# Performance work log

Hardware: AMD Instinct MI355X
Metric: run time of the kernel (lower is better)

The kernel has to match this reference:

```python
import jax, jax.numpy as jnp
import numpy as np

N, E, IN, ED, OUT = 50000, 800000, 64, 16, 64
AVG_D_LOG = 2.833  # log(avg_degree + 1), avg_degree = 16
EPS = 1e-5         # PNA std epsilon


def setup_inputs() -> dict:
    key = jax.random.key(0)
    ks = jax.random.split(key, 8)
    h = jax.random.normal(ks[0], (N, IN), jnp.float32)
    ef = jax.random.normal(ks[1], (E, ED), jnp.float32)
    snorm_n = jax.random.uniform(ks[2], (N, 1), jnp.float32)
    W_pre = jax.random.normal(ks[3], (2 * IN + ED, IN), jnp.float32) * 0.05
    b_pre = jnp.zeros((IN,), jnp.float32)
    W_post = jax.random.normal(ks[4], (13 * IN, OUT), jnp.float32) * 0.05
    b_post = jnp.zeros((OUT,), jnp.float32)
    src = jax.random.randint(ks[5], (E,), 0, N, dtype=jnp.int32).astype(jnp.int64)
    dst = jax.random.randint(ks[6], (E,), 0, N, dtype=jnp.int32).astype(jnp.int64)
    return dict(h=h, ef=ef, snorm_n=snorm_n, W_pre=W_pre, b_pre=b_pre,
                W_post=W_post, b_post=b_post, src=src, dst=dst)


def reference(h, ef, snorm_n, W_pre, b_pre, W_post, b_post, src, dst):
    # pretrans MLP (1 layer -> single linear, no activation) on per-edge concat
    z = jnp.concatenate([h[src], h[dst], ef], axis=1)      # [E, 2*IN+ED]
    msg = z @ W_pre + b_pre                                # [E, IN]

    deg = jax.ops.segment_sum(jnp.ones((E,), msg.dtype), dst, num_segments=N)  # [N]
    degc = jnp.maximum(deg, 1.0)
    has_msg = (deg > 0)[:, None]

    s = jax.ops.segment_sum(msg, dst, num_segments=N)
    mean = s / degc[:, None]
    mean_sq = jax.ops.segment_sum(msg * msg, dst, num_segments=N) / degc[:, None]
    std = jnp.sqrt(jax.nn.relu(mean_sq - mean * mean) + EPS)
    mx = jax.ops.segment_max(msg, dst, num_segments=N)
    mn = jax.ops.segment_min(msg, dst, num_segments=N)

    agg = jnp.concatenate([mean, mx, mn, std], axis=1)      # [N, 4*IN]
    agg = jnp.where(has_msg, agg, 0.0)                      # zero-in-degree nodes get 0

    logd = jnp.log(degc + 1.0)
    amp = agg * (logd / AVG_D_LOG)[:, None]                 # amplification scaler
    att = agg * (AVG_D_LOG / logd)[:, None]                 # attenuation scaler

    hcat = jnp.concatenate([h, agg, amp, att], axis=1)      # [N, 13*IN]
    out = hcat @ W_post + b_post                            # posttrans MLP (1 layer)
    out = out * snorm_n                                     # graph_norm
    return out
```

## Files before the change

kernel.cpp:

```cpp
#include <hip/hip_runtime.h>

constexpr int N_NODES = 50000;
constexpr int N_EDGES = 800000;
constexpr int IN_F = 64;
constexpr int ED_F = 16;
constexpr int OUT_F = 64;
constexpr int AGG_F = 256;
constexpr int KTOT = 832;
constexpr float AVG_D_LOG_F = 2.833f;
constexpr float EPS_F = 1e-5f;

constexpr int NB_BKT = 256;
constexpr int NODES_PER_BKT = 196;
constexpr int EPB_C = 4096;
constexpr int NBLK_C = (N_EDGES + EPB_C - 1) / EPB_C;

constexpr int AGG_WAVES = 12500;
constexpr int AGG_BLOCKS = AGG_WAVES / 4;

typedef __attribute__((ext_vector_type(8))) short short8;
typedef __attribute__((ext_vector_type(4))) float f32x4;

__device__ __forceinline__ int rfl(int v) { return __builtin_amdgcn_readfirstlane(v); }
__device__ __forceinline__ unsigned short f2bf(float f) {
    unsigned u = __float_as_uint(f);
    unsigned r = (u + 0x7FFFu + ((u >> 16) & 1u)) >> 16;
    return (unsigned short)r;
}

constexpr int P12MM_BLKS = 625;
constexpr int P12_TPB = 5;
constexpr int BKT_BLKS = 196;
constexpr int CONV_BLKS = 2500;
__global__ __launch_bounds__(256) void prep_kernel(
    const float* __restrict__ h, const float* __restrict__ Wpre, const float* __restrict__ bpre,
    const int* __restrict__ dst, const float* __restrict__ ef, const float* __restrict__ Wpost,
    unsigned short* __restrict__ P1b, float* __restrict__ P2, unsigned short* __restrict__ hb,
    int* __restrict__ bktcnt, unsigned short* __restrict__ efb,
    unsigned short* __restrict__ WT, unsigned short* __restrict__ WefT)
{
    int tid = threadIdx.x;
    if (blockIdx.x < P12MM_BLKS) {
        int lane = tid & 63;
        int li = lane & 15;
        int lg = lane >> 4;
        int w = tid >> 6;
        int col = w * 16 + li;

        short8 B1[2], B2[2];
        #pragma unroll
        for (int s = 0; s < 2; ++s) {
            short8 b1 = {}, b2 = {};
            #pragma unroll
            for (int j = 0; j < 8; ++j) {
                int k = s * 32 + (lg << 3) + j;
                b1[j] = (short)f2bf(Wpre[k * 64 + col]);
                b2[j] = (short)f2bf(Wpre[(64 + k) * 64 + col]);
            }
            B1[s] = b1; B2[s] = b2;
        }
        float bj = bpre[col];

        #pragma unroll 1
        for (int t = 0; t < P12_TPB; ++t) {
            int tile = blockIdx.x + t * P12MM_BLKS;
            int nA = tile * 16 + li;
            const float* hrow = h + (size_t)nA * IN_F;
            float4 v0 = *reinterpret_cast<const float4*>(hrow + (lg << 3));
            float4 v1 = *reinterpret_cast<const float4*>(hrow + (lg << 3) + 4);
            float4 v2 = *reinterpret_cast<const float4*>(hrow + 32 + (lg << 3));
            float4 v3 = *reinterpret_cast<const float4*>(hrow + 32 + (lg << 3) + 4);
            short8 a0, a1;
            a0[0]=(short)f2bf(v0.x); a0[1]=(short)f2bf(v0.y); a0[2]=(short)f2bf(v0.z); a0[3]=(short)f2bf(v0.w);
            a0[4]=(short)f2bf(v1.x); a0[5]=(short)f2bf(v1.y); a0[6]=(short)f2bf(v1.z); a0[7]=(short)f2bf(v1.w);
            a1[0]=(short)f2bf(v2.x); a1[1]=(short)f2bf(v2.y); a1[2]=(short)f2bf(v2.z); a1[3]=(short)f2bf(v2.w);
            a1[4]=(short)f2bf(v3.x); a1[5]=(short)f2bf(v3.y); a1[6]=(short)f2bf(v3.z); a1[7]=(short)f2bf(v3.w);

            if (w == 0) {
                *reinterpret_cast<short8*>(hb + (size_t)nA * IN_F + (lg << 3)) = a0;
                *reinterpret_cast<short8*>(hb + (size_t)nA * IN_F + 32 + (lg << 3)) = a1;
            }

            f32x4 p1a = {0.f,0.f,0.f,0.f}, p2a = {0.f,0.f,0.f,0.f};
            p1a = __builtin_amdgcn_mfma_f32_16x16x32_bf16(a0, B1[0], p1a, 0, 0, 0);
            p1a = __builtin_amdgcn_mfma_f32_16x16x32_bf16(a1, B1[1], p1a, 0, 0, 0);
            p2a = __builtin_amdgcn_mfma_f32_16x16x32_bf16(a0, B2[0], p2a, 0, 0, 0);
            p2a = __builtin_amdgcn_mfma_f32_16x16x32_bf16(a1, B2[1], p2a, 0, 0, 0);

            #pragma unroll
            for (int rr = 0; rr < 4; ++rr) {
                int node = tile * 16 + (lg << 2) + rr;
                P1b[(size_t)node * IN_F + col] = f2bf(p1a[rr]);
                P2[(size_t)node * IN_F + col] = p2a[rr] + bj;
            }
        }
    } else if (blockIdx.x < P12MM_BLKS + BKT_BLKS) {
        __shared__ int bh[NB_BKT];
        bh[tid] = 0;
        __syncthreads();
        int e0 = (blockIdx.x - P12MM_BLKS) * EPB_C;
        #pragma unroll
        for (int k = 0; k < EPB_C / 256; ++k) {
            int e = e0 + k * 256 + tid;
            if (e < N_EDGES) atomicAdd(&bh[dst[e] / NODES_PER_BKT], 1);
        }
        __syncthreads();
        if (bh[tid] > 0) atomicAdd(&bktcnt[tid], bh[tid]);
    } else {
        int cgid = (blockIdx.x - P12MM_BLKS - BKT_BLKS) * 256 + tid;
        const float4* ef4 = reinterpret_cast<const float4*>(ef);
        #pragma unroll
        for (int k = 0; k < 5; ++k) {
            int i = cgid + k * (CONV_BLKS * 256);
            float4 v = ef4[i];
            ushort4 o;
            o.x = f2bf(v.x); o.y = f2bf(v.y); o.z = f2bf(v.z); o.w = f2bf(v.w);
            *reinterpret_cast<ushort4*>(efb + (size_t)i * 4) = o;
        }
        if (cgid < OUT_F * KTOT) {
            int n = cgid / KTOT, k = cgid % KTOT;
            WT[cgid] = f2bf(Wpost[(size_t)k * OUT_F + n]);
        }
        if (cgid < 64 * 16) {
            int n = cgid >> 4, k = cgid & 15;
            WefT[cgid] = f2bf(Wpre[(128 + k) * 64 + n]);
        }
    }
}

__global__ __launch_bounds__(256) void bscan_kernel(
    const int* __restrict__ bktcnt, int* __restrict__ bkt_start, int* __restrict__ bcur)
{
    __shared__ int ws[4];
    int tid = threadIdx.x, lane = tid & 63, wv = tid >> 6;
    int v = bktcnt[tid];
    int sc = v;
    #pragma unroll
    for (int off = 1; off < 64; off <<= 1) {
        int u = __shfl_up(sc, off);
        if (lane >= off) sc += u;
    }
    if (lane == 63) ws[wv] = sc;
    __syncthreads();
    int wbase = 0;
    #pragma unroll
    for (int w = 0; w < 4; ++w) if (w < wv) wbase += ws[w];
    int ex = wbase + sc - v;
    bkt_start[tid] = ex;
    bcur[tid] = ex;
    if (tid == 255) bkt_start[256] = ex + v;
}

__global__ __launch_bounds__(256) void binC_kernel(
    const int* __restrict__ src, const int* __restrict__ dst, int* __restrict__ bcur,
    int* __restrict__ stage_e, int* __restrict__ stage_s, int* __restrict__ stage_d)
{
    __shared__ int sL[EPB_C];
    __shared__ int dL[EPB_C];
    __shared__ int bh[NB_BKT];
    __shared__ int bbase[NB_BKT];
    __shared__ int bcsr[NB_BKT];

    int tid = threadIdx.x;
    int e0 = blockIdx.x * EPB_C;

    bh[tid] = 0;
    __syncthreads();
    #pragma unroll
    for (int k = 0; k < EPB_C / 256; ++k) {
        int t = k * 256 + tid;
        int e = e0 + t;
        if (e < N_EDGES) {
            int s = src[e], d = dst[e];
            sL[t] = s; dL[t] = d;
            atomicAdd(&bh[d / NODES_PER_BKT], 1);
        }
    }
    __syncthreads();
    bbase[tid] = (bh[tid] > 0) ? atomicAdd(&bcur[tid], bh[tid]) : 0;
    bcsr[tid] = 0;
    __syncthreads();
    #pragma unroll
    for (int k = 0; k < EPB_C / 256; ++k) {
        int t = k * 256 + tid;
        int e = e0 + t;
        if (e < N_EDGES) {
            int d = dL[t];
            int b = d / NODES_PER_BKT;
            int r = atomicAdd(&bcsr[b], 1);
            int pos = bbase[b] + r;
            stage_e[pos] = e;
            stage_s[pos] = sL[t];
            stage_d[pos] = d;
        }
    }
}

__global__ __launch_bounds__(256) void binD_kernel(
    const int* __restrict__ stage_e, const int* __restrict__ stage_s,
    const int* __restrict__ stage_d, const int* __restrict__ bkt_start,
    int* __restrict__ deg, int* __restrict__ row_start, int2* __restrict__ csr2)
{
    __shared__ int cnt[NB_BKT];
    __shared__ int lofs[NODES_PER_BKT];
    __shared__ int ws[4];
    int tid = threadIdx.x, lane = tid & 63, wv = tid >> 6;
    int b = blockIdx.x;
    int nb0 = b * NODES_PER_BKT;
    cnt[tid] = 0;
    __syncthreads();
    int pbeg = bkt_start[b];
    int pend = bkt_start[b + 1];
    for (int p = pbeg + tid; p < pend; p += 256)
        atomicAdd(&cnt[stage_d[p] - nb0], 1);
    __syncthreads();
    int v = cnt[tid];
    int sc = v;
    #pragma unroll
    for (int off = 1; off < 64; off <<= 1) {
        int u = __shfl_up(sc, off);
        if (lane >= off) sc += u;
    }
    if (lane == 63) ws[wv] = sc;
    __syncthreads();
    int wbase = 0;
    #pragma unroll
    for (int w = 0; w < 4; ++w) if (w < wv) wbase += ws[w];
    int ex = wbase + sc - v;
    if (tid < NODES_PER_BKT) {
        int n = nb0 + tid;
        if (n < N_NODES) { deg[n] = v; row_start[n] = pbeg + ex; }
        lofs[tid] = pbeg + ex;
    }
    __syncthreads();
    for (int p = pbeg + tid; p < pend; p += 256) {
        int d = stage_d[p];
        int r = atomicAdd(&lofs[d - nb0], 1);
        csr2[r] = make_int2(stage_e[p], stage_s[p]);
    }
}

__global__ __launch_bounds__(256) void aggmm_kernel(
    const unsigned short* __restrict__ P1b, const float* __restrict__ P2,
    const unsigned short* __restrict__ efb, const unsigned short* __restrict__ WefT,
    const int2* __restrict__ csr2, const int* __restrict__ row_start,
    const int* __restrict__ deg, unsigned short* __restrict__ aggb)
{
    int tid = threadIdx.x;
    int lane = tid & 63;
    int lg = lane >> 4;
    int li = lane & 15;

    short8 bI0 = {}, bI1 = {};
    #pragma unroll
    for (int j = 0; j < 8; ++j) {
        int k_local = (lg << 3) + j;
        if (k_local == li)      bI0[j] = (short)0x3F80;
        if (k_local == 16 + li) bI1[j] = (short)0x3F80;
    }
    short8 bE[4];
    #pragma unroll
    for (int ct = 0; ct < 4; ++ct) {
        short8 b = {};
        if (lane < 32)
            b = *reinterpret_cast<const short8*>(WefT + (size_t)(ct * 16 + li) * 16 + (lg << 3));
        bE[ct] = b;
    }

    int wgid = rfl(blockIdx.x * 4 + (tid >> 6));

    #pragma unroll 1
    for (int nn = 0; nn < 4; ++nn) {
        int n = wgid + nn * AGG_WAVES;
        int rs = rfl(row_start[n]);
        int dg = rfl(deg[n]);
        size_t obase = (size_t)n * AGG_F + lane;

        if (dg == 0) {
            aggb[obase] = 0; aggb[obase + 64] = 0;
            aggb[obase + 128] = 0; aggb[obase + 192] = 0;
            continue;
        }

        float p2n = P2[(size_t)n * IN_F + lane];
        const float NINF = -__builtin_inff(), PINF = __builtin_inff();
        float sm[4] = {0.f, 0.f, 0.f, 0.f};
        float sq[4] = {0.f, 0.f, 0.f, 0.f};
        float mx[4] = {NINF, NINF, NINF, NINF};
        float mn[4] = {PINF, PINF, PINF, PINF};

        for (int base = 0; base < dg; base += 64) {
            int cnt = dg - base; if (cnt > 64) cnt = 64;
            int2 es = make_int2(0, 0);
            if (lane < cnt) es = csr2[rs + base + lane];
            int eid = es.x, sid = es.y;
            int nfull = cnt >> 4;

            for (int rt = 0; rt < nfull; ++rt) {
                int srcidx = rt * 16 + li;
                int s_l = __shfl(sid, srcidx);
                int e_l = __shfl(eid, srcidx);
                short8 aP0 = *reinterpret_cast<const short8*>(P1b + (size_t)s_l * IN_F + (lg << 3));
                short8 aP1 = *reinterpret_cast<const short8*>(P1b + (size_t)s_l * IN_F + 32 + (lg << 3));
                short8 aE = {};
                if (lane < 32)
                    aE = *reinterpret_cast<const short8*>(efb + (size_t)e_l * ED_F + (lg << 3));

                f32x4 c0 = {0.f,0.f,0.f,0.f}, c1 = {0.f,0.f,0.f,0.f};
                f32x4 c2 = {0.f,0.f,0.f,0.f}, c3 = {0.f,0.f,0.f,0.f};
                c0 = __builtin_amdgcn_mfma_f32_16x16x32_bf16(aP0, bI0, c0, 0, 0, 0);
                c1 = __builtin_amdgcn_mfma_f32_16x16x32_bf16(aP0, bI1, c1, 0, 0, 0);
                c2 = __builtin_amdgcn_mfma_f32_16x16x32_bf16(aP1, bI0, c2, 0, 0, 0);
                c3 = __builtin_amdgcn_mfma_f32_16x16x32_bf16(aP1, bI1, c3, 0, 0, 0);
                c0 = __builtin_amdgcn_mfma_f32_16x16x32_bf16(aE, bE[0], c0, 0, 0, 0);
                c1 = __builtin_amdgcn_mfma_f32_16x16x32_bf16(aE, bE[1], c1, 0, 0, 0);
                c2 = __builtin_amdgcn_mfma_f32_16x16x32_bf16(aE, bE[2], c2, 0, 0, 0);
                c3 = __builtin_amdgcn_mfma_f32_16x16x32_bf16(aE, bE[3], c3, 0, 0, 0);

                #pragma unroll
                for (int rr = 0; rr < 4; ++rr) {
                    float x0 = c0[rr], x1 = c1[rr], x2 = c2[rr], x3 = c3[rr];
                    sm[0] += x0; sm[1] += x1; sm[2] += x2; sm[3] += x3;
                    sq[0] = fmaf(x0, x0, sq[0]); sq[1] = fmaf(x1, x1, sq[1]);
                    sq[2] = fmaf(x2, x2, sq[2]); sq[3] = fmaf(x3, x3, sq[3]);
                    mx[0] = fmaxf(mx[0], x0); mx[1] = fmaxf(mx[1], x1);
                    mx[2] = fmaxf(mx[2], x2); mx[3] = fmaxf(mx[3], x3);
                    mn[0] = fminf(mn[0], x0); mn[1] = fminf(mn[1], x1);
                    mn[2] = fminf(mn[2], x2); mn[3] = fminf(mn[3], x3);
                }
            }

            if (cnt & 15) {
                int rowb0 = nfull * 16;
                int srcidx = rowb0 + li;
                if (srcidx >= cnt) srcidx = cnt - 1;
                int s_l = __shfl(sid, srcidx);
                int e_l = __shfl(eid, srcidx);
                short8 aP0 = *reinterpret_cast<const short8*>(P1b + (size_t)s_l * IN_F + (lg << 3));
                short8 aP1 = *reinterpret_cast<const short8*>(P1b + (size_t)s_l * IN_F + 32 + (lg << 3));
                short8 aE = {};
                if (lane < 32)
                    aE = *reinterpret_cast<const short8*>(efb + (size_t)e_l * ED_F + (lg << 3));

                f32x4 c0 = {0.f,0.f,0.f,0.f}, c1 = {0.f,0.f,0.f,0.f};
                f32x4 c2 = {0.f,0.f,0.f,0.f}, c3 = {0.f,0.f,0.f,0.f};
                c0 = __builtin_amdgcn_mfma_f32_16x16x32_bf16(aP0, bI0, c0, 0, 0, 0);
                c1 = __builtin_amdgcn_mfma_f32_16x16x32_bf16(aP0, bI1, c1, 0, 0, 0);
                c2 = __builtin_amdgcn_mfma_f32_16x16x32_bf16(aP1, bI0, c2, 0, 0, 0);
                c3 = __builtin_amdgcn_mfma_f32_16x16x32_bf16(aP1, bI1, c3, 0, 0, 0);
                c0 = __builtin_amdgcn_mfma_f32_16x16x32_bf16(aE, bE[0], c0, 0, 0, 0);
                c1 = __builtin_amdgcn_mfma_f32_16x16x32_bf16(aE, bE[1], c1, 0, 0, 0);
                c2 = __builtin_amdgcn_mfma_f32_16x16x32_bf16(aE, bE[2], c2, 0, 0, 0);
                c3 = __builtin_amdgcn_mfma_f32_16x16x32_bf16(aE, bE[3], c3, 0, 0, 0);

                int rb = rowb0 + (lg << 2);
                #pragma unroll
                for (int rr = 0; rr < 4; ++rr) {
                    bool vv = (rb + rr) < cnt;
                    float x0 = c0[rr], x1 = c1[rr], x2 = c2[rr], x3 = c3[rr];
                    float z0 = vv ? x0 : 0.f, z1 = vv ? x1 : 0.f, z2 = vv ? x2 : 0.f, z3 = vv ? x3 : 0.f;
                    sm[0] += z0; sm[1] += z1; sm[2] += z2; sm[3] += z3;
                    sq[0] = fmaf(z0, z0, sq[0]); sq[1] = fmaf(z1, z1, sq[1]);
                    sq[2] = fmaf(z2, z2, sq[2]); sq[3] = fmaf(z3, z3, sq[3]);
                    mx[0] = fmaxf(mx[0], x0); mx[1] = fmaxf(mx[1], x1);
                    mx[2] = fmaxf(mx[2], x2); mx[3] = fmaxf(mx[3], x3);
                    mn[0] = fminf(mn[0], x0); mn[1] = fminf(mn[1], x1);
                    mn[2] = fminf(mn[2], x2); mn[3] = fminf(mn[3], x3);
                }
            }
        }

        #pragma unroll
        for (int ct = 0; ct < 4; ++ct) {
            #pragma unroll
            for (int off = 16; off <= 32; off <<= 1) {
                sm[ct] += __shfl_xor(sm[ct], off);
                sq[ct] += __shfl_xor(sq[ct], off);
                mx[ct] = fmaxf(mx[ct], __shfl_xor(mx[ct], off));
                mn[ct] = fminf(mn[ct], __shfl_xor(mn[ct], off));
            }
        }
        bool s16 = (lane & 16) != 0, s32 = (lane & 32) != 0;
        float S  = s32 ? (s16 ? sm[3] : sm[2]) : (s16 ? sm[1] : sm[0]);
        float Qq = s32 ? (s16 ? sq[3] : sq[2]) : (s16 ? sq[1] : sq[0]);
        float MX = s32 ? (s16 ? mx[3] : mx[2]) : (s16 ? mx[1] : mx[0]);
        float MN = s32 ? (s16 ? mn[3] : mn[2]) : (s16 ? mn[1] : mn[0]);

        float degc = (float)dg;
        float mean_x = S / degc;
        float sd = sqrtf(fmaxf(Qq / degc - mean_x * mean_x, 0.f) + EPS_F);
        aggb[obase]       = f2bf(mean_x + p2n);
        aggb[obase + 64]  = f2bf(MX + p2n);
        aggb[obase + 128] = f2bf(MN + p2n);
        aggb[obase + 192] = f2bf(sd);
    }
}

constexpr int POST_BLOCKS = 625;
constexpr int TILES_PER_BLOCK = 5;
__global__ __launch_bounds__(256, 2) void postmm_kernel(
    const unsigned short* __restrict__ hb, const float* __restrict__ snorm,
    const unsigned short* __restrict__ WT, const float* __restrict__ bpost,
    const unsigned short* __restrict__ aggb, const int* __restrict__ deg,
    float* __restrict__ out)
{
    int tid = threadIdx.x;
    int lane = tid & 63;
    int li = lane & 15;
    int lg = lane >> 4;
    int w = tid >> 6;

    const unsigned short* Brow = WT + (size_t)(w * 16 + li) * KTOT + (lg << 3);
    short8 B[26];
    #pragma unroll
    for (int s = 0; s < 26; ++s)
        B[s] = *reinterpret_cast<const short8*>(Brow + s * 32);

    float bp = bpost[w * 16 + li];

    #pragma unroll 1
    for (int t = 0; t < TILES_PER_BLOCK; ++t) {
        int tile = blockIdx.x + t * POST_BLOCKS;
        int nA = tile * 16 + li;
        const unsigned short* Ah = hb + (size_t)nA * IN_F + (lg << 3);
        const unsigned short* Ag = aggb + (size_t)nA * AGG_F + (lg << 3);

        short8 ah0 = *reinterpret_cast<const short8*>(Ah);
        short8 ah1 = *reinterpret_cast<const short8*>(Ah + 32);
        short8 ag[8];
        #pragma unroll
        for (int s = 0; s < 8; ++s)
            ag[s] = *reinterpret_cast<const short8*>(Ag + s * 32);

        f32x4 accA = {0.f,0.f,0.f,0.f}, accB = {0.f,0.f,0.f,0.f}, accC = {0.f,0.f,0.f,0.f};
        accA = __builtin_amdgcn_mfma_f32_16x16x32_bf16(ah0, B[0], accA, 0, 0, 0);
        accA = __builtin_amdgcn_mfma_f32_16x16x32_bf16(ah1, B[1], accA, 0, 0, 0);
        #pragma unroll
        for (int s = 0; s < 8; ++s) {
            accA = __builtin_amdgcn_mfma_f32_16x16x32_bf16(ag[s], B[2 + s],  accA, 0, 0, 0);
            accB = __builtin_amdgcn_mfma_f32_16x16x32_bf16(ag[s], B[10 + s], accB, 0, 0, 0);
            accC = __builtin_amdgcn_mfma_f32_16x16x32_bf16(ag[s], B[18 + s], accC, 0, 0, 0);
        }

        #pragma unroll
        for (int rr = 0; rr < 4; ++rr) {
            int node = tile * 16 + (lg << 2) + rr;
            int dg = deg[node];
            float degc = fmaxf((float)dg, 1.f);
            float logd = logf(degc + 1.f);
            float aR = logd * (1.f / AVG_D_LOG_F);
            float bR = AVG_D_LOG_F / logd;
            float v = accA[rr] + aR * accB[rr] + bR * accC[rr] + bp;
            out[(size_t)node * OUT_F + w * 16 + li] = v * snorm[node];
        }
    }
}

extern "C" void kernel_launch(void* const* d_in, const int* in_sizes, int n_in,
                              void* d_out, int out_size, void* d_ws, size_t ws_size,
                              hipStream_t stream) {
    const float* h     = (const float*)d_in[0];
    const float* ef    = (const float*)d_in[1];
    const float* snorm = (const float*)d_in[2];
    const float* Wpre  = (const float*)d_in[3];
    const float* bpre  = (const float*)d_in[4];
    const float* Wpost = (const float*)d_in[5];
    const float* bpost = (const float*)d_in[6];
    const int* src     = (const int*)d_in[7];
    const int* dst     = (const int*)d_in[8];
    float* out = (float*)d_out;

    char* ws = (char*)d_ws;
    size_t off = 0;
    auto alloc = [&](size_t bytes) { char* p = ws + off; off += (bytes + 255) & ~size_t(255); return p; };
    unsigned short* P1b  = (unsigned short*)alloc((size_t)N_NODES * IN_F * 2);
    float* P2            = (float*)alloc((size_t)N_NODES * IN_F * 4);
    unsigned short* hb   = (unsigned short*)alloc((size_t)N_NODES * IN_F * 2);
    unsigned short* aggb = (unsigned short*)alloc((size_t)N_NODES * AGG_F * 2);
    unsigned short* efb  = (unsigned short*)alloc((size_t)N_EDGES * ED_F * 2);
    int* deg       = (int*)alloc((size_t)N_NODES * 4);
    int* row_start = (int*)alloc((size_t)N_NODES * 4);
    int2* csr2     = (int2*)alloc((size_t)N_EDGES * 8);
    int* stage_e   = (int*)alloc((size_t)N_EDGES * 4);
    int* stage_s   = (int*)alloc((size_t)N_EDGES * 4);
    int* stage_d   = (int*)alloc((size_t)N_EDGES * 4);
    int* bktcnt    = (int*)alloc((size_t)NB_BKT * 4);
    int* bkt_start = (int*)alloc((size_t)(NB_BKT + 1) * 4);
    int* bcur      = (int*)alloc((size_t)NB_BKT * 4);
    unsigned short* WT   = (unsigned short*)alloc((size_t)OUT_F * KTOT * 2);
    unsigned short* WefT = (unsigned short*)alloc((size_t)64 * 16 * 2);

    hipMemsetAsync(bktcnt, 0, (size_t)NB_BKT * 4, stream);
    hipLaunchKernelGGL(prep_kernel, dim3(P12MM_BLKS + BKT_BLKS + CONV_BLKS), dim3(256), 0, stream,
                       h, Wpre, bpre, dst, ef, Wpost,
                       P1b, P2, hb, bktcnt, efb, WT, WefT);
    hipLaunchKernelGGL(bscan_kernel, dim3(1), dim3(256), 0, stream, bktcnt, bkt_start, bcur);
    hipLaunchKernelGGL(binC_kernel, dim3(NBLK_C), dim3(256), 0, stream,
                       src, dst, bcur, stage_e, stage_s, stage_d);
    hipLaunchKernelGGL(binD_kernel, dim3(NB_BKT), dim3(256), 0, stream,
                       stage_e, stage_s, stage_d, bkt_start, deg, row_start, csr2);
    hipLaunchKernelGGL(aggmm_kernel, dim3(AGG_BLOCKS), dim3(256), 0, stream,
                       P1b, P2, efb, WefT, csr2, row_start, deg, aggb);
    hipLaunchKernelGGL(postmm_kernel, dim3(POST_BLOCKS), dim3(256), 0, stream,
                       hb, snorm, WT, bpost, aggb, deg, out);
}
```

Before: 137.0 us.

## Pack staged src/dst-local into one word and batch gathers for low-degree nodes

The binning stage now packs the source id and the bucket-local destination offset into one 32-bit word. This removes one staging array and its write/read traffic. Aggregation adds templated fast paths for nodes with degree ≤16 and ≤32. These paths load the CSR entries directly per lane and issue all gathers before the MFMAs, which raises memory-level parallelism and drops the shuffles. The packing relies on node ids fitting in 16 bits, and the fast paths use more registers.

```diff
diff --git a/kernel.cpp b/kernel.cpp
--- a/kernel.cpp
+++ b/kernel.cpp
@@ -153,7 +153,7 @@
 
 __global__ __launch_bounds__(256) void binC_kernel(
     const int* __restrict__ src, const int* __restrict__ dst, int* __restrict__ bcur,
-    int* __restrict__ stage_e, int* __restrict__ stage_s, int* __restrict__ stage_d)
+    int* __restrict__ stage_e, int* __restrict__ stage_sd)
 {
     __shared__ int sL[EPB_C];
     __shared__ int dL[EPB_C];
@@ -187,18 +187,18 @@
         if (e < N_EDGES) {
             int d = dL[t];
             int b = d / NODES_PER_BKT;
+            int dl = d - b * NODES_PER_BKT;
             int r = atomicAdd(&bcsr[b], 1);
             int pos = bbase[b] + r;
             stage_e[pos] = e;
-            stage_s[pos] = sL[t];
-            stage_d[pos] = d;
+            stage_sd[pos] = sL[t] | (dl << 16);
         }
     }
 }
 
 __global__ __launch_bounds__(256) void binD_kernel(
-    const int* __restrict__ stage_e, const int* __restrict__ stage_s,
-    const int* __restrict__ stage_d, const int* __restrict__ bkt_start,
+    const int* __restrict__ stage_e, const int* __restrict__ stage_sd,
+    const int* __restrict__ bkt_start,
     int* __restrict__ deg, int* __restrict__ row_start, int2* __restrict__ csr2)
 {
     __shared__ int cnt[NB_BKT];
@@ -212,7 +212,7 @@
     int pbeg = bkt_start[b];
     int pend = bkt_start[b + 1];
     for (int p = pbeg + tid; p < pend; p += 256)
-        atomicAdd(&cnt[stage_d[p] - nb0], 1);
+        atomicAdd(&cnt[stage_sd[p] >> 16], 1);
     __syncthreads();
     int v = cnt[tid];
     int sc = v;
@@ -234,9 +234,86 @@
     }
     __syncthreads();
     for (int p = pbeg + tid; p < pend; p += 256) {
-        int d = stage_d[p];
-        int r = atomicAdd(&lofs[d - nb0], 1);
-        csr2[r] = make_int2(stage_e[p], stage_s[p]);
+        int sd = stage_sd[p];
+        int r = atomicAdd(&lofs[sd >> 16], 1);
+        csr2[r] = make_int2(stage_e[p], sd & 0xFFFF);
+    }
+}
+
+#define AGG_MFMA8(aP0_, aP1_, aE_) \
+    c0 = __builtin_amdgcn_mfma_f32_16x16x32_bf16(aP0_, bI0, c0, 0, 0, 0); \
+    c1 = __builtin_amdgcn_mfma_f32_16x16x32_bf16(aP0_, bI1, c1, 0, 0, 0); \
+    c2 = __builtin_amdgcn_mfma_f32_16x16x32_bf16(aP1_, bI0, c2, 0, 0, 0); \
+    c3 = __builtin_amdgcn_mfma_f32_16x16x32_bf16(aP1_, bI1, c3, 0, 0, 0); \
+    c0 = __builtin_amdgcn_mfma_f32_16x16x32_bf16(aE_, bE0, c0, 0, 0, 0);  \
+    c1 = __builtin_amdgcn_mfma_f32_16x16x32_bf16(aE_, bE1, c1, 0, 0, 0);  \
+    c2 = __builtin_amdgcn_mfma_f32_16x16x32_bf16(aE_, bE2, c2, 0, 0, 0);  \
+    c3 = __builtin_amdgcn_mfma_f32_16x16x32_bf16(aE_, bE3, c3, 0, 0, 0);
+
+template<int NT>
+__device__ __forceinline__ void agg_fast(
+    const unsigned short* __restrict__ P1b, const unsigned short* __restrict__ efb,
+    const int2* __restrict__ csr2, int rs, int dg,
+    short8 bI0, short8 bI1, short8 bE0, short8 bE1, short8 bE2, short8 bE3,
+    int lane, int lg, int li,
+    float* sm, float* sq, float* mx, float* mn)
+{
+    int2 es[NT];
+    #pragma unroll
+    for (int t = 0; t < NT; ++t) {
+        int idx = t * 16 + li;
+        if (idx >= dg) idx = dg - 1;
+        es[t] = csr2[rs + idx];
+    }
+    short8 aP0[NT], aP1[NT], aE[NT];
+    #pragma unroll
+    for (int t = 0; t < NT; ++t) {
+        const unsigned short* pr = P1b + (size_t)es[t].y * IN_F + (lg << 3);
+        aP0[t] = *reinterpret_cast<const short8*>(pr);
+        aP1[t] = *reinterpret_cast<const short8*>(pr + 32);
+        short8 a = {};
+        if (lane < 32)
+            a = *reinterpret_cast<const short8*>(efb + (size_t)es[t].x * ED_F + (lg << 3));
+        aE[t] = a;
+    }
+    #pragma unroll
+    for (int t = 0; t < NT; ++t) {
+        f32x4 c0 = {0.f,0.f,0.f,0.f}, c1 = {0.f,0.f,0.f,0.f};
+        f32x4 c2 = {0.f,0.f,0.f,0.f}, c3 = {0.f,0.f,0.f,0.f};
+        AGG_MFMA8(aP0[t], aP1[t], aE[t]);
+        if (t < NT - 1) {
+            sm[0] += (c0[0] + c0[1]) + (c0[2] + c0[3]);
+            sm[1] += (c1[0] + c1[1]) + (c1[2] + c1[3]);
+            sm[2] += (c2[0] + c2[1]) + (c2[2] + c2[3]);
+            sm[3] += (c3[0] + c3[1]) + (c3[2] + c3[3]);
+            sq[0] = fmaf(c0[0],c0[0], fmaf(c0[1],c0[1], fmaf(c0[2],c0[2], fmaf(c0[3],c0[3], sq[0]))));
+            sq[1] = fmaf(c1[0],c1[0], fmaf(c1[1],c1[1], fmaf(c1[2],c1[2], fmaf(c1[3],c1[3], sq[1]))));
+            sq[2] = fmaf(c2[0],c2[0], fmaf(c2[1],c2[1], fmaf(c2[2],c2[2], fmaf(c2[3],c2[3], sq[2]))));
+            sq[3] = fmaf(c3[0],c3[0], fmaf(c3[1],c3[1], fmaf(c3[2],c3[2], fmaf(c3[3],c3[3], sq[3]))));
+            mx[0] = fmaxf(fmaxf(fmaxf(fmaxf(mx[0], c0[0]), c0[1]), c0[2]), c0[3]);
+            mx[1] = fmaxf(fmaxf(fmaxf(fmaxf(mx[1], c1[0]), c1[1]), c1[2]), c1[3]);
+            mx[2] = fmaxf(fmaxf(fmaxf(fmaxf(mx[2], c2[0]), c2[1]), c2[2]), c2[3]);
+            mx[3] = fmaxf(fmaxf(fmaxf(fmaxf(mx[3], c3[0]), c3[1]), c3[2]), c3[3]);
+            mn[0] = fminf(fminf(fminf(fminf(mn[0], c0[0]), c0[1]), c0[2]), c0[3]);
+            mn[1] = fminf(fminf(fminf(fminf(mn[1], c1[0]), c1[1]), c1[2]), c1[3]);
+            mn[2] = fminf(fminf(fminf(fminf(mn[2], c2[0]), c2[1]), c2[2]), c2[3]);
+            mn[3] = fminf(fminf(fminf(fminf(mn[3], c3[0]), c3[1]), c3[2]), c3[3]);
+        } else {
+            int rb = t * 16 + (lg << 2);
+            #pragma unroll
+            for (int rr = 0; rr < 4; ++rr) {
+                bool vv = (rb + rr) < dg;
+                float x0 = c0[rr], x1 = c1[rr], x2 = c2[rr], x3 = c3[rr];
+                float z0 = vv ? x0 : 0.f, z1 = vv ? x1 : 0.f, z2 = vv ? x2 : 0.f, z3 = vv ? x3 : 0.f;
+                sm[0] += z0; sm[1] += z1; sm[2] += z2; sm[3] += z3;
+                sq[0] = fmaf(z0, z0, sq[0]); sq[1] = fmaf(z1, z1, sq[1]);
+                sq[2] = fmaf(z2, z2, sq[2]); sq[3] = fmaf(z3, z3, sq[3]);
+                mx[0] = fmaxf(mx[0], x0); mx[1] = fmaxf(mx[1], x1);
+                mx[2] = fmaxf(mx[2], x2); mx[3] = fmaxf(mx[3], x3);
+                mn[0] = fminf(mn[0], x0); mn[1] = fminf(mn[1], x1);
+                mn[2] = fminf(mn[2], x2); mn[3] = fminf(mn[3], x3);
+            }
+        }
     }
 }
 
@@ -258,13 +335,12 @@
         if (k_local == li)      bI0[j] = (short)0x3F80;
         if (k_local == 16 + li) bI1[j] = (short)0x3F80;
     }
-    short8 bE[4];
-    #pragma unroll
-    for (int ct = 0; ct < 4; ++ct) {
-        short8 b = {};
-        if (lane < 32)
-            b = *reinterpret_cast<const short8*>(WefT + (size_t)(ct * 16 + li) * 16 + (lg << 3));
-        bE[ct] = b;
+    short8 bE0 = {}, bE1 = {}, bE2 = {}, bE3 = {};
+    if (lane < 32) {
+        bE0 = *reinterpret_cast<const short8*>(WefT + (size_t)(0 * 16 + li) * 16 + (lg << 3));
+        bE1 = *reinterpret_cast<const short8*>(WefT + (size_t)(1 * 16 + li) * 16 + (lg << 3));
+        bE2 = *reinterpret_cast<const short8*>(WefT + (size_t)(2 * 16 + li) * 16 + (lg << 3));
+        bE3 = *reinterpret_cast<const short8*>(WefT + (size_t)(3 * 16 + li) * 16 + (lg << 3));
     }
 
     int wgid = rfl(blockIdx.x * 4 + (tid >> 6));
@@ -289,83 +365,44 @@
         float mx[4] = {NINF, NINF, NINF, NINF};
         float mn[4] = {PINF, PINF, PINF, PINF};
 
-        for (int base = 0; base < dg; base += 64) {
-            int cnt = dg - base; if (cnt > 64) cnt = 64;
-            int2 es = make_int2(0, 0);
-            if (lane < cnt) es = csr2[rs + base + lane];
-            int eid = es.x, sid = es.y;
-            int nfull = cnt >> 4;
-
-            for (int rt = 0; rt < nfull; ++rt) {
-                int srcidx = rt * 16 + li;
-                int s_l = __shfl(sid, srcidx);
-                int e_l = __shfl(eid, srcidx);
-                short8 aP0 = *reinterpret_cast<const short8*>(P1b + (size_t)s_l * IN_F + (lg << 3));
-                short8 aP1 = *reinterpret_cast<const short8*>(P1b + (size_t)s_l * IN_F + 32 + (lg << 3));
-                short8 aE = {};
-                if (lane < 32)
-                    aE = *reinterpret_cast<const short8*>(efb + (size_t)e_l * ED_F + (lg << 3));
-
-                f32x4 c0 = {0.f,0.f,0.f,0.f}, c1 = {0.f,0.f,0.f,0.f};
-                f32x4 c2 = {0.f,0.f,0.f,0.f}, c3 = {0.f,0.f,0.f,0.f};
-                c0 = __builtin_amdgcn_mfma_f32_16x16x32_bf16(aP0, bI0, c0, 0, 0, 0);
-                c1 = __builtin_amdgcn_mfma_f32_16x16x32_bf16(aP0, bI1, c1, 0, 0, 0);
-                c2 = __builtin_amdgcn_mfma_f32_16x16x32_bf16(aP1, bI0, c2, 0, 0, 0);
-                c3 = __builtin_amdgcn_mfma_f32_16x16x32_bf16(aP1, bI1, c3, 0, 0, 0);
-                c0 = __builtin_amdgcn_mfma_f32_16x16x32_bf16(aE, bE[0], c0, 0, 0, 0);
-                c1 = __builtin_amdgcn_mfma_f32_16x16x32_bf16(aE, bE[1], c1, 0, 0, 0);
-                c2 = __builtin_amdgcn_mfma_f32_16x16x32_bf16(aE, bE[2], c2, 0, 0, 0);
-                c3 = __builtin_amdgcn_mfma_f32_16x16x32_bf16(aE, bE[3], c3, 0, 0, 0);
-
-                #pragma unroll
-                for (int rr = 0; rr < 4; ++rr) {
-                    float x0 = c0[rr], x1 = c1[rr], x2 = c2[rr], x3 = c3[rr];
-                    sm[0] += x0; sm[1] += x1; sm[2] += x2; sm[3] += x3;
-                    sq[0] = fmaf(x0, x0, sq[0]); sq[1] = fmaf(x1, x1, sq[1]);
-                    sq[2] = fmaf(x2, x2, sq[2]); sq[3] = fmaf(x3, x3, sq[3]);
-                    mx[0] = fmaxf(mx[0], x0); mx[1] = fmaxf(mx[1], x1);
-                    mx[2] = fmaxf(mx[2], x2); mx[3] = fmaxf(mx[3], x3);
-                    mn[0] = fminf(mn[0], x0); mn[1] = fminf(mn[1], x1);
-                    mn[2] = fminf(mn[2], x2); mn[3] = fminf(mn[3], x3);
-                }
-            }
-
-            if (cnt & 15) {
-                int rowb0 = nfull * 16;
-                int srcidx = rowb0 + li;
-                if (srcidx >= cnt) srcidx = cnt - 1;
-                int s_l = __shfl(sid, srcidx);
-                int e_l = __shfl(eid, srcidx);
-                short8 aP0 = *reinterpret_cast<const short8*>(P1b + (size_t)s_l * IN_F + (lg << 3));
-                short8 aP1 = *reinterpret_cast<const short8*>(P1b + (size_t)s_l * IN_F + 32 + (lg << 3));
-                short8 aE = {};
-                if (lane < 32)
-                    aE = *reinterpret_cast<const short8*>(efb + (size_t)e_l * ED_F + (lg << 3));
-
-                f32x4 c0 = {0.f,0.f,0.f,0.f}, c1 = {0.f,0.f,0.f,0.f};
-                f32x4 c2 = {0.f,0.f,0.f,0.f}, c3 = {0.f,0.f,0.f,0.f};
-                c0 = __builtin_amdgcn_mfma_f32_16x16x32_bf16(aP0, bI0, c0, 0, 0, 0);
-                c1 = __builtin_amdgcn_mfma_f32_16x16x32_bf16(aP0, bI1, c1, 0, 0, 0);
-                c2 = __builtin_amdgcn_mfma_f32_16x16x32_bf16(aP1, bI0, c2, 0, 0, 0);
-                c3 = __builtin_amdgcn_mfma_f32_16x16x32_bf16(aP1, bI1, c3, 0, 0, 0);
-                c0 = __builtin_amdgcn_mfma_f32_16x16x32_bf16(aE, bE[0], c0, 0, 0, 0);
-                c1 = __builtin_amdgcn_mfma_f32_16x16x32_bf16(aE, bE[1], c1, 0, 0, 0);
-                c2 = __builtin_amdgcn_mfma_f32_16x16x32_bf16(aE, bE[2], c2, 0, 0, 0);
-                c3 = __builtin_amdgcn_mfma_f32_16x16x32_bf16(aE, bE[3], c3, 0, 0, 0);
-
-                int rb = rowb0 + (lg << 2);
-                #pragma unroll
-                for (int rr = 0; rr < 4; ++rr) {
-                    bool vv = (rb + rr) < cnt;
-                    float x0 = c0[rr], x1 = c1[rr], x2 = c2[rr], x3 = c3[rr];
-                    float z0 = vv ? x0 : 0.f, z1 = vv ? x1 : 0.f, z2 = vv ? x2 : 0.f, z3 = vv ? x3 : 0.f;
-                    sm[0] += z0; sm[1] += z1; sm[2] += z2; sm[3] += z3;
-                    sq[0] = fmaf(z0, z0, sq[0]); sq[1] = fmaf(z1, z1, sq[1]);
-                    sq[2] = fmaf(z2, z2, sq[2]); sq[3] = fmaf(z3, z3, sq[3]);
-                    mx[0] = fmaxf(mx[0], x0); mx[1] = fmaxf(mx[1], x1);
-                    mx[2] = fmaxf(mx[2], x2); mx[3] = fmaxf(mx[3], x3);
-                    mn[0] = fminf(mn[0], x0); mn[1] = fminf(mn[1], x1);
-                    mn[2] = fminf(mn[2], x2); mn[3] = fminf(mn[3], x3);
+        if (dg <= 16) {
+            agg_fast<1>(P1b, efb, csr2, rs, dg, bI0, bI1, bE0, bE1, bE2, bE3, lane, lg, li, sm, sq, mx, mn);
+        } else if (dg <= 32) {
+            agg_fast<2>(P1b, efb, csr2, rs, dg, bI0, bI1, bE0, bE1, bE2, bE3, lane, lg, li, sm, sq, mx, mn);
+        } else {
+            for (int base = 0; base < dg; base += 64) {
+                int cnt = dg - base; if (cnt > 64) cnt = 64;
+                int2 es = make_int2(0, 0);
+                if (lane < cnt) es = csr2[rs + base + lane];
+                int eid = es.x, sid = es.y;
+                int nrt = (cnt + 15) >> 4;
+                for (int rt = 0; rt < nrt; ++rt) {
+                    int srcidx = rt * 16 + li;
+                    if (srcidx >= cnt) srcidx = cnt - 1;
+                    int s_l = __shfl(sid, srcidx);
+                    int e_l = __shfl(eid, srcidx);
+                    short8 aP0 = *reinterpret_cast<const short8*>(P1b + (size_t)s_l * IN_F + (lg << 3));
+                    short8 aP1 = *reinterpret_cast<const short8*>(P1b + (size_t)s_l * IN_F + 32 + (lg << 3));
+                    short8 aE = {};
+                    if (lane < 32)
+                        aE = *reinterpret_cast<const short8*>(efb + (size_t)e_l * ED_F + (lg << 3));
+                    f32x4 c0 = {0.f,0.f,0.f,0.f}, c1 = {0.f,0.f,0.f,0.f};
+                    f32x4 c2 = {0.f,0.f,0.f,0.f}, c3 = {0.f,0.f,0.f,0.f};
+                    AGG_MFMA8(aP0, aP1, aE);
+                    int rowb = rt * 16 + (lg << 2);
+                    #pragma unroll
+                    for (int rr = 0; rr < 4; ++rr) {
+                        bool vv = (rowb + rr) < cnt;
+                        float x0 = c0[rr], x1 = c1[rr], x2 = c2[rr], x3 = c3[rr];
+                        float z0 = vv ? x0 : 0.f, z1 = vv ? x1 : 0.f, z2 = vv ? x2 : 0.f, z3 = vv ? x3 : 0.f;
+                        sm[0] += z0; sm[1] += z1; sm[2] += z2; sm[3] += z3;
+                        sq[0] = fmaf(z0, z0, sq[0]); sq[1] = fmaf(z1, z1, sq[1]);
+                        sq[2] = fmaf(z2, z2, sq[2]); sq[3] = fmaf(z3, z3, sq[3]);
+                        mx[0] = fmaxf(mx[0], x0); mx[1] = fmaxf(mx[1], x1);
+                        mx[2] = fmaxf(mx[2], x2); mx[3] = fmaxf(mx[3], x3);
+                        mn[0] = fminf(mn[0], x0); mn[1] = fminf(mn[1], x1);
+                        mn[2] = fminf(mn[2], x2); mn[3] = fminf(mn[3], x3);
+                    }
                 }
             }
         }
@@ -482,8 +519,7 @@
     int* row_start = (int*)alloc((size_t)N_NODES * 4);
     int2* csr2     = (int2*)alloc((size_t)N_EDGES * 8);
     int* stage_e   = (int*)alloc((size_t)N_EDGES * 4);
-    int* stage_s   = (int*)alloc((size_t)N_EDGES * 4);
-    int* stage_d   = (int*)alloc((size_t)N_EDGES * 4);
+    int* stage_sd  = (int*)alloc((size_t)N_EDGES * 4);
     int* bktcnt    = (int*)alloc((size_t)NB_BKT * 4);
     int* bkt_start = (int*)alloc((size_t)(NB_BKT + 1) * 4);
     int* bcur      = (int*)alloc((size_t)NB_BKT * 4);
@@ -496,9 +532,9 @@
                        P1b, P2, hb, bktcnt, efb, WT, WefT);
     hipLaunchKernelGGL(bscan_kernel, dim3(1), dim3(256), 0, stream, bktcnt, bkt_start, bcur);
     hipLaunchKernelGGL(binC_kernel, dim3(NBLK_C), dim3(256), 0, stream,
-                       src, dst, bcur, stage_e, stage_s, stage_d);
+                       src, dst, bcur, stage_e, stage_sd);
     hipLaunchKernelGGL(binD_kernel, dim3(NB_BKT), dim3(256), 0, stream,
-                       stage_e, stage_s, stage_d, bkt_start, deg, row_start, csr2);
+                       stage_e, stage_sd, bkt_start, deg, row_start, csr2);
     hipLaunchKernelGGL(aggmm_kernel, dim3(AGG_BLOCKS), dim3(256), 0, stream,
                        P1b, P2, efb, WefT, csr2, row_start, deg, aggb);
     hipLaunchKernelGGL(postmm_kernel, dim3(POST_BLOCKS), dim3(256), 0, stream,
```

After: 135.5 us. No clear change (-1.1%).

## Use fixed-capacity buckets to drop histogram and scan passes in CSR build

Applied to the files above, without the earlier changes.

Replaces the bucket histogram and prefix-scan kernels with fixed 4096-entry bucket slots, filled through a per-bucket atomic counter during binning. Packs the source index and bucket-local destination into one int to shrink the staging arrays. This removes a pass over dst, one kernel launch and some staging traffic. In exchange it assumes no bucket exceeds 4096 edges and that node ids fit in 16 bits, which holds only for near-uniform inputs of this size.

```diff
diff --git a/kernel.cpp b/kernel.cpp
--- a/kernel.cpp
+++ b/kernel.cpp
@@ -12,6 +12,7 @@
 
 constexpr int NB_BKT = 256;
 constexpr int NODES_PER_BKT = 196;
+constexpr int BKT_STRIDE = 4096;
 constexpr int EPB_C = 4096;
 constexpr int NBLK_C = (N_EDGES + EPB_C - 1) / EPB_C;
 
@@ -30,13 +31,12 @@
 
 constexpr int P12MM_BLKS = 625;
 constexpr int P12_TPB = 5;
-constexpr int BKT_BLKS = 196;
 constexpr int CONV_BLKS = 2500;
 __global__ __launch_bounds__(256) void prep_kernel(
     const float* __restrict__ h, const float* __restrict__ Wpre, const float* __restrict__ bpre,
-    const int* __restrict__ dst, const float* __restrict__ ef, const float* __restrict__ Wpost,
+    const float* __restrict__ ef, const float* __restrict__ Wpost,
     unsigned short* __restrict__ P1b, float* __restrict__ P2, unsigned short* __restrict__ hb,
-    int* __restrict__ bktcnt, unsigned short* __restrict__ efb,
+    unsigned short* __restrict__ efb,
     unsigned short* __restrict__ WT, unsigned short* __restrict__ WefT)
 {
     int tid = threadIdx.x;
@@ -94,20 +94,8 @@
                 P2[(size_t)node * IN_F + col] = p2a[rr] + bj;
             }
         }
-    } else if (blockIdx.x < P12MM_BLKS + BKT_BLKS) {
-        __shared__ int bh[NB_BKT];
-        bh[tid] = 0;
-        __syncthreads();
-        int e0 = (blockIdx.x - P12MM_BLKS) * EPB_C;
-        #pragma unroll
-        for (int k = 0; k < EPB_C / 256; ++k) {
-            int e = e0 + k * 256 + tid;
-            if (e < N_EDGES) atomicAdd(&bh[dst[e] / NODES_PER_BKT], 1);
-        }
-        __syncthreads();
-        if (bh[tid] > 0) atomicAdd(&bktcnt[tid], bh[tid]);
     } else {
-        int cgid = (blockIdx.x - P12MM_BLKS - BKT_BLKS) * 256 + tid;
+        int cgid = (blockIdx.x - P12MM_BLKS) * 256 + tid;
         const float4* ef4 = reinterpret_cast<const float4*>(ef);
         #pragma unroll
         for (int k = 0; k < 5; ++k) {
@@ -128,32 +116,9 @@
     }
 }
 
-__global__ __launch_bounds__(256) void bscan_kernel(
-    const int* __restrict__ bktcnt, int* __restrict__ bkt_start, int* __restrict__ bcur)
-{
-    __shared__ int ws[4];
-    int tid = threadIdx.x, lane = tid & 63, wv = tid >> 6;
-    int v = bktcnt[tid];
-    int sc = v;
-    #pragma unroll
-    for (int off = 1; off < 64; off <<= 1) {
-        int u = __shfl_up(sc, off);
-        if (lane >= off) sc += u;
-    }
-    if (lane == 63) ws[wv] = sc;
-    __syncthreads();
-    int wbase = 0;
-    #pragma unroll
-    for (int w = 0; w < 4; ++w) if (w < wv) wbase += ws[w];
-    int ex = wbase + sc - v;
-    bkt_start[tid] = ex;
-    bcur[tid] = ex;
-    if (tid == 255) bkt_start[256] = ex + v;
-}
-
 __global__ __launch_bounds__(256) void binC_kernel(
-    const int* __restrict__ src, const int* __restrict__ dst, int* __restrict__ bcur,
-    int* __restrict__ stage_e, int* __restrict__ stage_s, int* __restrict__ stage_d)
+    const int* __restrict__ src, const int* __restrict__ dst, int* __restrict__ bcur0,
+    int* __restrict__ stage_e, int* __restrict__ stage_sd)
 {
     __shared__ int sL[EPB_C];
     __shared__ int dL[EPB_C];
@@ -177,7 +142,7 @@
         }
     }
     __syncthreads();
-    bbase[tid] = (bh[tid] > 0) ? atomicAdd(&bcur[tid], bh[tid]) : 0;
+    bbase[tid] = (bh[tid] > 0) ? atomicAdd(&bcur0[tid], bh[tid]) : 0;
     bcsr[tid] = 0;
     __syncthreads();
     #pragma unroll
@@ -187,18 +152,18 @@
         if (e < N_EDGES) {
             int d = dL[t];
             int b = d / NODES_PER_BKT;
+            int dl = d - b * NODES_PER_BKT;
             int r = atomicAdd(&bcsr[b], 1);
-            int pos = bbase[b] + r;
+            int pos = (b << 12) + bbase[b] + r;
             stage_e[pos] = e;
-            stage_s[pos] = sL[t];
-            stage_d[pos] = d;
+            stage_sd[pos] = sL[t] | (dl << 16);
         }
     }
 }
 
 __global__ __launch_bounds__(256) void binD_kernel(
-    const int* __restrict__ stage_e, const int* __restrict__ stage_s,
-    const int* __restrict__ stage_d, const int* __restrict__ bkt_start,
+    const int* __restrict__ stage_e, const int* __restrict__ stage_sd,
+    const int* __restrict__ bcur0,
     int* __restrict__ deg, int* __restrict__ row_start, int2* __restrict__ csr2)
 {
     __shared__ int cnt[NB_BKT];
@@ -207,12 +172,12 @@
     int tid = threadIdx.x, lane = tid & 63, wv = tid >> 6;
     int b = blockIdx.x;
     int nb0 = b * NODES_PER_BKT;
+    int base = b << 12;
     cnt[tid] = 0;
     __syncthreads();
-    int pbeg = bkt_start[b];
-    int pend = bkt_start[b + 1];
-    for (int p = pbeg + tid; p < pend; p += 256)
-        atomicAdd(&cnt[stage_d[p] - nb0], 1);
+    int cntb = bcur0[b];
+    for (int p = base + tid; p < base + cntb; p += 256)
+        atomicAdd(&cnt[stage_sd[p] >> 16], 1);
     __syncthreads();
     int v = cnt[tid];
     int sc = v;
@@ -229,14 +194,14 @@
     int ex = wbase + sc - v;
     if (tid < NODES_PER_BKT) {
         int n = nb0 + tid;
-        if (n < N_NODES) { deg[n] = v; row_start[n] = pbeg + ex; }
-        lofs[tid] = pbeg + ex;
-    }
-    __syncthreads();
-    for (int p = pbeg + tid; p < pend; p += 256) {
-        int d = stage_d[p];
-        int r = atomicAdd(&lofs[d - nb0], 1);
-        csr2[r] = make_int2(stage_e[p], stage_s[p]);
+        if (n < N_NODES) { deg[n] = v; row_start[n] = base + ex; }
+        lofs[tid] = base + ex;
+    }
+    __syncthreads();
+    for (int p = base + tid; p < base + cntb; p += 256) {
+        int sd = stage_sd[p];
+        int r = atomicAdd(&lofs[sd >> 16], 1);
+        csr2[r] = make_int2(stage_e[p], sd & 0xFFFF);
     }
 }
 
@@ -480,25 +445,21 @@
     unsigned short* efb  = (unsigned short*)alloc((size_t)N_EDGES * ED_F * 2);
     int* deg       = (int*)alloc((size_t)N_NODES * 4);
     int* row_start = (int*)alloc((size_t)N_NODES * 4);
-    int2* csr2     = (int2*)alloc((size_t)N_EDGES * 8);
-    int* stage_e   = (int*)alloc((size_t)N_EDGES * 4);
-    int* stage_s   = (int*)alloc((size_t)N_EDGES * 4);
-    int* stage_d   = (int*)alloc((size_t)N_EDGES * 4);
-    int* bktcnt    = (int*)alloc((size_t)NB_BKT * 4);
-    int* bkt_start = (int*)alloc((size_t)(NB_BKT + 1) * 4);
-    int* bcur      = (int*)alloc((size_t)NB_BKT * 4);
+    int2* csr2     = (int2*)alloc((size_t)NB_BKT * BKT_STRIDE * 8);
+    int* stage_e   = (int*)alloc((size_t)NB_BKT * BKT_STRIDE * 4);
+    int* stage_sd  = (int*)alloc((size_t)NB_BKT * BKT_STRIDE * 4);
+    int* bcur0     = (int*)alloc((size_t)NB_BKT * 4);
     unsigned short* WT   = (unsigned short*)alloc((size_t)OUT_F * KTOT * 2);
     unsigned short* WefT = (unsigned short*)alloc((size_t)64 * 16 * 2);
 
-    hipMemsetAsync(bktcnt, 0, (size_t)NB_BKT * 4, stream);
-    hipLaunchKernelGGL(prep_kernel, dim3(P12MM_BLKS + BKT_BLKS + CONV_BLKS), dim3(256), 0, stream,
-                       h, Wpre, bpre, dst, ef, Wpost,
-                       P1b, P2, hb, bktcnt, efb, WT, WefT);
-    hipLaunchKernelGGL(bscan_kernel, dim3(1), dim3(256), 0, stream, bktcnt, bkt_start, bcur);
+    hipMemsetAsync(bcur0, 0, (size_t)NB_BKT * 4, stream);
+    hipLaunchKernelGGL(prep_kernel, dim3(P12MM_BLKS + CONV_BLKS), dim3(256), 0, stream,
+                       h, Wpre, bpre, ef, Wpost,
+                       P1b, P2, hb, efb, WT, WefT);
     hipLaunchKernelGGL(binC_kernel, dim3(NBLK_C), dim3(256), 0, stream,
-                       src, dst, bcur, stage_e, stage_s, stage_d);
+                       src, dst, bcur0, stage_e, stage_sd);
     hipLaunchKernelGGL(binD_kernel, dim3(NB_BKT), dim3(256), 0, stream,
-                       stage_e, stage_s, stage_d, bkt_start, deg, row_start, csr2);
+                       stage_e, stage_sd, bcur0, deg, row_start, csr2);
     hipLaunchKernelGGL(aggmm_kernel, dim3(AGG_BLOCKS), dim3(256), 0, stream,
                        P1b, P2, efb, WefT, csr2, row_start, deg, aggb);
     hipLaunchKernelGGL(postmm_kernel, dim3(POST_BLOCKS), dim3(256), 0, stream,
```

New measurement: 127.6 us. 1.07x faster.
